# Performance work log

Hardware: AMD Instinct MI355X
Metric: run time of the kernel (lower is better)

## Reference

```python
import jax, jax.numpy as jnp
import numpy as np

B, T, D, H = 2, 2048, 1024, 16
DH = D // H

def setup_inputs() -> dict:
    key = jax.random.key(0)
    ks = jax.random.split(key, 6)
    s = 0.02
    return {
        "x": jax.random.normal(ks[0], (B, T, D), jnp.float32),
        "Wq": jax.random.normal(ks[1], (D, D), jnp.float32) * s,
        "Wk": jax.random.normal(ks[2], (D, D), jnp.float32) * s,
        "Wv": jax.random.normal(ks[3], (D, D), jnp.float32) * s,
        "Wo": jax.random.normal(ks[4], (D, D), jnp.float32) * s,
        "bo": jnp.zeros((D,), jnp.float32),
    }

def reference(x, Wq, Wk, Wv, Wo, bo):
    Bx, Tx, _ = x.shape
    # project and split heads: [B, H, T, DH]
    q = (x @ Wq).reshape(Bx, Tx, H, DH).transpose(0, 2, 1, 3)
    k = (x @ Wk).reshape(Bx, Tx, H, DH).transpose(0, 2, 1, 3)
    v = (x @ Wv).reshape(Bx, Tx, H, DH).transpose(0, 2, 1, 3)
    scores = jnp.einsum("bhqd,bhkd->bhqk", q, k)  # [B,H,T,T]
    causal = jnp.triu(jnp.ones((Tx, Tx), bool), k=1)  # True above diagonal
    scores = jnp.where(causal, -jnp.inf, scores)
    # original scales AFTER masking (equivalent math)
    w = jax.nn.softmax(scores / jnp.sqrt(jnp.float32(DH)), axis=-1)
    # dropout p=0.0 -> identity
    ctx = jnp.einsum("bhqk,bhkd->bhqd", w, v)
    ctx = ctx.transpose(0, 2, 1, 3).reshape(Bx, Tx, D)
    return ctx @ Wo + bo
```

## Files before the change

kernel.cpp:

```cpp
#include <hip/hip_runtime.h>
#include <hip/hip_bf16.h>


typedef __bf16 bf16x8 __attribute__((ext_vector_type(8)));
typedef __bf16 bf16x4 __attribute__((ext_vector_type(4)));
typedef float  f32x4  __attribute__((ext_vector_type(4)));

#define Bx 2
#define Tx 2048
#define Dx 1024
#define Hx 16
#define DHx 64

__global__ __launch_bounds__(256) void prep(const float* __restrict__ x,
                                            const float* __restrict__ W0,
                                            const float* __restrict__ W1,
                                            const float* __restrict__ W2,
                                            const float* __restrict__ W3,
                                            __bf16* __restrict__ xb,
                                            __bf16* __restrict__ Wt) {
    const int z = blockIdx.z;
    if (z == 0) {
        const int blk = blockIdx.y * 16 + blockIdx.x;
        const float* xp = x + (size_t)blk * 16384;
        __bf16* xo = xb + (size_t)blk * 16384;
#pragma unroll
        for (int i = 0; i < 16; i++) {
            float4 v = *(const float4*)(xp + i * 1024 + threadIdx.x * 4);
            bf16x4 o;
            o[0] = (__bf16)v.x; o[1] = (__bf16)v.y; o[2] = (__bf16)v.z; o[3] = (__bf16)v.w;
            *(bf16x4*)(xo + i * 1024 + threadIdx.x * 4) = o;
        }
        return;
    }
    __shared__ float tile[64][65];
    const float* W = (z == 1) ? W0 : (z == 2) ? W1 : (z == 3) ? W2 : W3;
    __bf16* o = Wt + (size_t)(z - 1) * Dx * Dx;
    int k0 = blockIdx.x * 64, n0 = blockIdx.y * 64;
    int t = threadIdx.x;
    int cc = t & 63, rbase = t >> 6;
#pragma unroll
    for (int i = 0; i < 16; i++) {
        int rr = rbase + i * 4;
        tile[rr][cc] = W[(size_t)(k0 + rr) * Dx + n0 + cc];
    }
    __syncthreads();
#pragma unroll
    for (int i = 0; i < 16; i++) {
        int rr = rbase + i * 4;
        o[(size_t)(n0 + rr) * Dx + k0 + cc] = (__bf16)tile[cc][rr];
    }
}

static __device__ __forceinline__ void gload16(const __bf16* g, __bf16* l) {
    __builtin_amdgcn_global_load_lds((const __attribute__((address_space(1))) void*)g,
                                     (__attribute__((address_space(3))) void*)l, 16, 0, 0);
}

__global__ __launch_bounds__(256, 6) void gemm_qkv(const __bf16* __restrict__ A,
                                                   const __bf16* __restrict__ BT,
                                                   __bf16* __restrict__ Qb,
                                                   __bf16* __restrict__ Kb,
                                                   __bf16* __restrict__ Vt) {
    __shared__ __bf16 As[64 * 32];
    __shared__ __bf16 Bs[128 * 32];
    const int t = threadIdx.x;
    const int lane = t & 63, wave = t >> 6;
    const int lane15 = lane & 15, quad = lane >> 4;
    const int m0 = blockIdx.x * 64, n0 = blockIdx.y * 128;
    const int wm = wave & 1, wn = wave >> 1;

    const int srA = wave * 16 + (lane >> 2), sc = (lane & 3) * 8;
    const int srB = wave * 32 + (lane >> 2);
    const __bf16* Ag = A + (size_t)(m0 + srA) * Dx + sc;
    const __bf16* Bg = BT + (size_t)(n0 + srB) * Dx + sc;
    __bf16* Asl  = As + (wave * 16) * 32;
    __bf16* Bsl0 = Bs + (wave * 32) * 32;
    __bf16* Bsl1 = Bs + (wave * 32 + 16) * 32;

    f32x4 acc[2][4];
#pragma unroll
    for (int i = 0; i < 2; i++)
#pragma unroll
        for (int j = 0; j < 4; j++) acc[i][j] = (f32x4){0.f, 0.f, 0.f, 0.f};

    for (int k0 = 0; k0 < Dx; k0 += 32) {
        gload16(Ag, Asl);
        gload16(Bg, Bsl0);
        gload16(Bg + 16 * Dx, Bsl1);
        Ag += 32; Bg += 32;
        __syncthreads();
        bf16x8 af[2], bf[4];
#pragma unroll
        for (int i = 0; i < 2; i++)
            af[i] = *(const bf16x8*)&As[(wm * 32 + i * 16 + lane15) * 32 + quad * 8];
#pragma unroll
        for (int j = 0; j < 4; j++)
            bf[j] = *(const bf16x8*)&Bs[(wn * 64 + j * 16 + lane15) * 32 + quad * 8];
#pragma unroll
        for (int mt = 0; mt < 2; mt++)
#pragma unroll
            for (int nt = 0; nt < 4; nt++)
                acc[mt][nt] = __builtin_amdgcn_mfma_f32_16x16x32_bf16(af[mt], bf[nt], acc[mt][nt], 0, 0, 0);
        __syncthreads();
    }

    const int z = n0 >> 10;
    if (z < 2) {
        __bf16* outp = z ? Kb : Qb;
        const float scale = z ? 1.0f : 0.125f;
#pragma unroll
        for (int mt = 0; mt < 2; mt++)
#pragma unroll
            for (int nt = 0; nt < 4; nt++) {
                const int cc = (n0 + wn * 64 + nt * 16 + lane15) & 1023;
                const int h = cc >> 6, dh = cc & 63;
#pragma unroll
                for (int r4 = 0; r4 < 4; r4++) {
                    const int row = m0 + wm * 32 + mt * 16 + quad * 4 + r4;
                    const int b = row >> 11, tt = row & 2047;
                    outp[(((size_t)(b * Hx + h) * Tx + tt) << 6) + dh] =
                        (__bf16)(acc[mt][nt][r4] * scale);
                }
            }
    } else {
#pragma unroll
        for (int mt = 0; mt < 2; mt++)
#pragma unroll
            for (int nt = 0; nt < 4; nt++) {
                const int cc = (n0 + wn * 64 + nt * 16 + lane15) & 1023;
                const int h = cc >> 6, dh = cc & 63;
#pragma unroll
                for (int r4 = 0; r4 < 4; r4++) {
                    const int row = m0 + wm * 32 + mt * 16 + quad * 4 + r4;
                    const int b = row >> 11, tt = row & 2047;
                    Vt[((size_t)(b * Hx + h) * DHx + dh) * Tx + tt] = (__bf16)acc[mt][nt][r4];
                }
            }
    }
}

__global__ __launch_bounds__(256, 4) void gemm_out(const __bf16* __restrict__ A,
                                                   const __bf16* __restrict__ BT,
                                                   float* __restrict__ outf,
                                                   const float* __restrict__ bias) {
    __shared__ __bf16 As[64 * 32];
    __shared__ __bf16 Bs[64 * 32];
    const int t = threadIdx.x;
    const int lane = t & 63, wave = t >> 6;
    const int lane15 = lane & 15, quad = lane >> 4;
    const int m0 = blockIdx.x * 64, n0 = blockIdx.y * 64;
    const int wm = wave & 1, wn = wave >> 1;

    const int sr = wave * 16 + (lane >> 2), sc = (lane & 3) * 8;
    const __bf16* Ag = A + (size_t)(m0 + sr) * Dx + sc;
    const __bf16* Bg = BT + (size_t)(n0 + sr) * Dx + sc;
    __bf16* Asl = As + (wave * 16) * 32;
    __bf16* Bsl = Bs + (wave * 16) * 32;

    f32x4 acc[2][2];
#pragma unroll
    for (int i = 0; i < 2; i++)
#pragma unroll
        for (int j = 0; j < 2; j++) acc[i][j] = (f32x4){0.f, 0.f, 0.f, 0.f};

    for (int k0 = 0; k0 < Dx; k0 += 32) {
        gload16(Ag, Asl);
        gload16(Bg, Bsl);
        Ag += 32; Bg += 32;
        __syncthreads();
        bf16x8 af[2], bf[2];
#pragma unroll
        for (int i = 0; i < 2; i++) {
            af[i] = *(const bf16x8*)&As[(wm * 32 + i * 16 + lane15) * 32 + quad * 8];
            bf[i] = *(const bf16x8*)&Bs[(wn * 32 + i * 16 + lane15) * 32 + quad * 8];
        }
#pragma unroll
        for (int mt = 0; mt < 2; mt++)
#pragma unroll
            for (int nt = 0; nt < 2; nt++)
                acc[mt][nt] = __builtin_amdgcn_mfma_f32_16x16x32_bf16(af[mt], bf[nt], acc[mt][nt], 0, 0, 0);
        __syncthreads();
    }

#pragma unroll
    for (int mt = 0; mt < 2; mt++)
#pragma unroll
        for (int nt = 0; nt < 2; nt++) {
            const int col = n0 + wn * 32 + nt * 16 + lane15;
#pragma unroll
            for (int r4 = 0; r4 < 4; r4++) {
                const int row = m0 + wm * 32 + mt * 16 + quad * 4 + r4;
                outf[(size_t)row * Dx + col] = acc[mt][nt][r4] + bias[col];
            }
        }
}

__global__ __launch_bounds__(512) void attn_mfma(const __bf16* __restrict__ Q,
                                                 const __bf16* __restrict__ K,
                                                 const __bf16* __restrict__ Vt,
                                                 __bf16* __restrict__ ctx) {
    __shared__ __bf16 Ks[64 * 72];
    __shared__ __bf16 Vs[64 * 72];
    __shared__ __bf16 Ps[128 * 80];
    const int t = threadIdx.x;
    const int lane = t & 63, wave = t >> 6;
    const int lane15 = lane & 15, quad = (lane >> 4) & 3;
    const int h = blockIdx.y, b = blockIdx.z;
    const size_t headoff = ((size_t)(b * Hx + h)) * Tx * DHx;
    const __bf16* Kbase = K + headoff;
    const __bf16* Vbase = Vt + headoff;
    const int sr = t >> 3, sc = (t & 7) * 8;

    for (int pass = 0; pass < 2; pass++) {
        const int chunk = pass ? (15 - blockIdx.x) : blockIdx.x;
        const int q0 = chunk * 128;
        const int ktiles = 2 * chunk + 2;
        const int qg = q0 + wave * 16 + quad * 4;

        bf16x8 qf0, qf1;
        {
            const __bf16* Qp = Q + headoff + (size_t)(q0 + wave * 16 + lane15) * 64 + quad * 8;
            qf0 = *(const bf16x8*)Qp;
            qf1 = *(const bf16x8*)(Qp + 32);
        }
        f32x4 o[4];
#pragma unroll
        for (int i = 0; i < 4; i++) o[i] = (f32x4){0.f, 0.f, 0.f, 0.f};
        float lpart[4] = {0.f, 0.f, 0.f, 0.f};

        bf16x8 kpre = *(const bf16x8*)(Kbase + (size_t)sr * 64 + sc);
        bf16x8 vpre = *(const bf16x8*)(Vbase + (size_t)sr * Tx + sc);

        for (int kt = 0; kt < ktiles; kt++) {
            __syncthreads();
            *(bf16x8*)&Ks[sr * 72 + sc] = kpre;
            *(bf16x8*)&Vs[sr * 72 + sc] = vpre;
            __syncthreads();
            if (kt + 1 < ktiles) {
                kpre = *(const bf16x8*)(Kbase + (size_t)((kt + 1) * 64 + sr) * 64 + sc);
                vpre = *(const bf16x8*)(Vbase + (size_t)sr * Tx + (kt + 1) * 64 + sc);
            }
            if (kt * 64 > q0 + wave * 16 + 15) continue;

            f32x4 s[4];
#pragma unroll
            for (int nt = 0; nt < 4; nt++) {
                s[nt] = (f32x4){0.f, 0.f, 0.f, 0.f};
                bf16x8 b0 = *(const bf16x8*)&Ks[(nt * 16 + lane15) * 72 + quad * 8];
                s[nt] = __builtin_amdgcn_mfma_f32_16x16x32_bf16(qf0, b0, s[nt], 0, 0, 0);
                bf16x8 b1 = *(const bf16x8*)&Ks[(nt * 16 + lane15) * 72 + 32 + quad * 8];
                s[nt] = __builtin_amdgcn_mfma_f32_16x16x32_bf16(qf1, b1, s[nt], 0, 0, 0);
            }

            const int kbase = kt * 64;
#pragma unroll
            for (int nt = 0; nt < 4; nt++)
#pragma unroll
                for (int reg = 0; reg < 4; reg++) {
                    float e = __expf(s[nt][reg]);
                    if (kbase + nt * 16 + lane15 > qg + reg) e = 0.f;
                    lpart[reg] += e;
                    Ps[(wave * 16 + quad * 4 + reg) * 80 + nt * 16 + lane15] = (__bf16)e;
                }

            bf16x8 pa0 = *(const bf16x8*)&Ps[(wave * 16 + lane15) * 80 + quad * 8];
            bf16x8 pa1 = *(const bf16x8*)&Ps[(wave * 16 + lane15) * 80 + 32 + quad * 8];
#pragma unroll
            for (int dt = 0; dt < 4; dt++) {
                bf16x8 vb0 = *(const bf16x8*)&Vs[(dt * 16 + lane15) * 72 + quad * 8];
                o[dt] = __builtin_amdgcn_mfma_f32_16x16x32_bf16(pa0, vb0, o[dt], 0, 0, 0);
                bf16x8 vb1 = *(const bf16x8*)&Vs[(dt * 16 + lane15) * 72 + 32 + quad * 8];
                o[dt] = __builtin_amdgcn_mfma_f32_16x16x32_bf16(pa1, vb1, o[dt], 0, 0, 0);
            }
        }

        float inv[4];
#pragma unroll
        for (int reg = 0; reg < 4; reg++) {
            float l = lpart[reg];
#pragma unroll
            for (int off = 1; off < 16; off <<= 1) l += __shfl_xor(l, off);
            inv[reg] = 1.f / l;
        }
#pragma unroll
        for (int dt = 0; dt < 4; dt++)
#pragma unroll
            for (int reg = 0; reg < 4; reg++) {
                int q = q0 + wave * 16 + quad * 4 + reg;
                ctx[(((size_t)(b * Tx + q)) * Hx + h) * 64 + dt * 16 + lane15] =
                    (__bf16)(o[dt][reg] * inv[reg]);
            }
    }
}

extern "C" void kernel_launch(void* const* d_in, const int* in_sizes, int n_in,
                              void* d_out, int out_size, void* d_ws, size_t ws_size,
                              hipStream_t stream) {
    const float* x  = (const float*)d_in[0];
    const float* Wq = (const float*)d_in[1];
    const float* Wk = (const float*)d_in[2];
    const float* Wv = (const float*)d_in[3];
    const float* Wo = (const float*)d_in[4];
    const float* bo = (const float*)d_in[5];
    float* out = (float*)d_out;

    char* ws = (char*)d_ws;
    __bf16* xb  = (__bf16*)(ws + 0);
    __bf16* Wt  = (__bf16*)(ws + (8ull << 20));
    __bf16* Qb  = (__bf16*)(ws + (16ull << 20));
    __bf16* Kb  = (__bf16*)(ws + (24ull << 20));
    __bf16* Vtg = (__bf16*)(ws + (32ull << 20));
    __bf16* ctx = (__bf16*)(ws + (40ull << 20));

    prep<<<dim3(16, 16, 5), 256, 0, stream>>>(x, Wq, Wk, Wv, Wo, xb, Wt);

    gemm_qkv<<<dim3(Bx * Tx / 64, 3 * Dx / 128), 256, 0, stream>>>(xb, Wt, Qb, Kb, Vtg);

    attn_mfma<<<dim3(Tx / 256, Hx, Bx), 512, 0, stream>>>(Qb, Kb, Vtg, ctx);

    gemm_out<<<dim3(Bx * Tx / 64, Dx / 64), 256, 0, stream>>>(ctx, Wt + 3 * (1u << 20), out, bo);
}
```

Measured before the change: 185.3 us.

## Shrink attention blocks to 64 queries and double-buffer K/V tiles in LDS

The attention kernel now uses 256-thread blocks that each handle 64-row query chunks, with two balanced passes per block, and launches twice as many blocks. K and V tiles are double-buffered in shared memory, so each iteration needs one barrier instead of two, and the next tile's global loads are issued before that barrier. The intent is to increase occupancy and parallelism and to cut synchronization stalls. In exchange there are more blocks that each reload K/V, more LDS per block, and a per-wave causal skip that is no longer present.

```diff
diff --git a/kernel.cpp b/kernel.cpp
--- a/kernel.cpp
+++ b/kernel.cpp
@@ -196,26 +196,26 @@
         }
 }
 
-__global__ __launch_bounds__(512) void attn_mfma(const __bf16* __restrict__ Q,
+__global__ __launch_bounds__(256) void attn_mfma(const __bf16* __restrict__ Q,
                                                  const __bf16* __restrict__ K,
                                                  const __bf16* __restrict__ Vt,
                                                  __bf16* __restrict__ ctx) {
-    __shared__ __bf16 Ks[64 * 72];
-    __shared__ __bf16 Vs[64 * 72];
-    __shared__ __bf16 Ps[128 * 80];
+    __shared__ __bf16 Ks[2][64 * 72];
+    __shared__ __bf16 Vs[2][64 * 72];
+    __shared__ __bf16 Ps[64 * 80];
     const int t = threadIdx.x;
     const int lane = t & 63, wave = t >> 6;
-    const int lane15 = lane & 15, quad = (lane >> 4) & 3;
+    const int lane15 = lane & 15, quad = lane >> 4;
     const int h = blockIdx.y, b = blockIdx.z;
     const size_t headoff = ((size_t)(b * Hx + h)) * Tx * DHx;
     const __bf16* Kbase = K + headoff;
     const __bf16* Vbase = Vt + headoff;
-    const int sr = t >> 3, sc = (t & 7) * 8;
+    const int sr = t >> 2, sc = (t & 3) * 16;
 
     for (int pass = 0; pass < 2; pass++) {
-        const int chunk = pass ? (15 - blockIdx.x) : blockIdx.x;
-        const int q0 = chunk * 128;
-        const int ktiles = 2 * chunk + 2;
+        const int chunk = pass ? (31 - blockIdx.x) : blockIdx.x;
+        const int q0 = chunk * 64;
+        const int ktiles = chunk + 1;
         const int qg = q0 + wave * 16 + quad * 4;
 
         bf16x8 qf0, qf1;
@@ -229,27 +229,35 @@
         for (int i = 0; i < 4; i++) o[i] = (f32x4){0.f, 0.f, 0.f, 0.f};
         float lpart[4] = {0.f, 0.f, 0.f, 0.f};
 
-        bf16x8 kpre = *(const bf16x8*)(Kbase + (size_t)sr * 64 + sc);
-        bf16x8 vpre = *(const bf16x8*)(Vbase + (size_t)sr * Tx + sc);
+        bf16x8 kpre0, kpre1, vpre0, vpre1;
+        {
+            const __bf16* Kp = Kbase + (size_t)sr * 64 + sc;
+            kpre0 = *(const bf16x8*)Kp; kpre1 = *(const bf16x8*)(Kp + 8);
+            const __bf16* Vp = Vbase + (size_t)sr * Tx + sc;
+            vpre0 = *(const bf16x8*)Vp; vpre1 = *(const bf16x8*)(Vp + 8);
+        }
 
         for (int kt = 0; kt < ktiles; kt++) {
+            const int cur = kt & 1;
+            *(bf16x8*)&Ks[cur][sr * 72 + sc] = kpre0;
+            *(bf16x8*)&Ks[cur][sr * 72 + sc + 8] = kpre1;
+            *(bf16x8*)&Vs[cur][sr * 72 + sc] = vpre0;
+            *(bf16x8*)&Vs[cur][sr * 72 + sc + 8] = vpre1;
+            if (kt + 1 < ktiles) {
+                const __bf16* Kp = Kbase + (size_t)((kt + 1) * 64 + sr) * 64 + sc;
+                kpre0 = *(const bf16x8*)Kp; kpre1 = *(const bf16x8*)(Kp + 8);
+                const __bf16* Vp = Vbase + (size_t)sr * Tx + (kt + 1) * 64 + sc;
+                vpre0 = *(const bf16x8*)Vp; vpre1 = *(const bf16x8*)(Vp + 8);
+            }
             __syncthreads();
-            *(bf16x8*)&Ks[sr * 72 + sc] = kpre;
-            *(bf16x8*)&Vs[sr * 72 + sc] = vpre;
-            __syncthreads();
-            if (kt + 1 < ktiles) {
-                kpre = *(const bf16x8*)(Kbase + (size_t)((kt + 1) * 64 + sr) * 64 + sc);
-                vpre = *(const bf16x8*)(Vbase + (size_t)sr * Tx + (kt + 1) * 64 + sc);
-            }
-            if (kt * 64 > q0 + wave * 16 + 15) continue;
 
             f32x4 s[4];
 #pragma unroll
             for (int nt = 0; nt < 4; nt++) {
                 s[nt] = (f32x4){0.f, 0.f, 0.f, 0.f};
-                bf16x8 b0 = *(const bf16x8*)&Ks[(nt * 16 + lane15) * 72 + quad * 8];
+                bf16x8 b0 = *(const bf16x8*)&Ks[cur][(nt * 16 + lane15) * 72 + quad * 8];
                 s[nt] = __builtin_amdgcn_mfma_f32_16x16x32_bf16(qf0, b0, s[nt], 0, 0, 0);
-                bf16x8 b1 = *(const bf16x8*)&Ks[(nt * 16 + lane15) * 72 + 32 + quad * 8];
+                bf16x8 b1 = *(const bf16x8*)&Ks[cur][(nt * 16 + lane15) * 72 + 32 + quad * 8];
                 s[nt] = __builtin_amdgcn_mfma_f32_16x16x32_bf16(qf1, b1, s[nt], 0, 0, 0);
             }
 
@@ -268,9 +276,9 @@
             bf16x8 pa1 = *(const bf16x8*)&Ps[(wave * 16 + lane15) * 80 + 32 + quad * 8];
 #pragma unroll
             for (int dt = 0; dt < 4; dt++) {
-                bf16x8 vb0 = *(const bf16x8*)&Vs[(dt * 16 + lane15) * 72 + quad * 8];
+                bf16x8 vb0 = *(const bf16x8*)&Vs[cur][(dt * 16 + lane15) * 72 + quad * 8];
                 o[dt] = __builtin_amdgcn_mfma_f32_16x16x32_bf16(pa0, vb0, o[dt], 0, 0, 0);
-                bf16x8 vb1 = *(const bf16x8*)&Vs[(dt * 16 + lane15) * 72 + 32 + quad * 8];
+                bf16x8 vb1 = *(const bf16x8*)&Vs[cur][(dt * 16 + lane15) * 72 + 32 + quad * 8];
                 o[dt] = __builtin_amdgcn_mfma_f32_16x16x32_bf16(pa1, vb1, o[dt], 0, 0, 0);
             }
         }
@@ -291,6 +299,7 @@
                 ctx[(((size_t)(b * Tx + q)) * Hx + h) * 64 + dt * 16 + lane15] =
                     (__bf16)(o[dt][reg] * inv[reg]);
             }
+        __syncthreads();
     }
 }
 
@@ -317,7 +326,7 @@
 
     gemm_qkv<<<dim3(Bx * Tx / 64, 3 * Dx / 128), 256, 0, stream>>>(xb, Wt, Qb, Kb, Vtg);
 
-    attn_mfma<<<dim3(Tx / 256, Hx, Bx), 512, 0, stream>>>(Qb, Kb, Vtg, ctx);
+    attn_mfma<<<dim3(Tx / 128, Hx, Bx), 256, 0, stream>>>(Qb, Kb, Vtg, ctx);
 
     gemm_out<<<dim3(Bx * Tx / 64, Dx / 64), 256, 0, stream>>>(ctx, Wt + 3 * (1u << 20), out, bo);
 }
```

Measured after the change: 187.1 us. About the same (+1.0%).
